# Performance work log

Hardware: AMD Instinct MI355X
Metric: run time of the kernel (lower is better)

Reference implementation:

```python
import jax, jax.numpy as jnp
import numpy as np

# Static ragged block structure: (num_graphs_in_bucket, n) -> block tensor (B, n, n, C)
BLOCKS = [(128, 32), (64, 48), (32, 64), (16, 96)]
C = 64
DEPTH = 2
EPS = 1e-5
N_TOTAL = sum(b * n * n for b, n in BLOCKS)  # 557056


def _mlp(h, w, b):
    # stack of DEPTH Linear(C->C) + ReLU layers (1x1 convs in the torch module)
    for d in range(w.shape[0]):
        h = jax.nn.relu(jnp.einsum('...i,oi->...o', h, w[d]) + b[d])
    return h


def _bn(h, g, b, m, v):
    # eval-mode BatchNorm1d with running stats
    return g * (h - m) * jax.lax.rsqrt(v + EPS) + b


def setup_inputs() -> dict:
    key = jax.random.key(0)
    ks = jax.random.split(key, 8)
    s = 1.0 / np.sqrt(C)

    def lin(k):
        return jax.random.normal(k, (C, C), jnp.float32) * s

    return dict(
        x=jax.random.normal(ks[0], (N_TOTAL, C), jnp.float32),
        w_m1=jax.random.normal(ks[1], (DEPTH, C, C), jnp.float32) * s,
        b_m1=jnp.zeros((DEPTH, C), jnp.float32),
        w_m2=jax.random.normal(ks[2], (DEPTH, C, C), jnp.float32) * s,
        b_m2=jnp.zeros((DEPTH, C), jnp.float32),
        W_skip=lin(ks[3]), b_skip=jnp.zeros((C,), jnp.float32),
        W_u1=lin(ks[4]), b_u1=jnp.zeros((C,), jnp.float32),
        g1=jnp.ones((C,), jnp.float32), beta1=jnp.zeros((C,), jnp.float32),
        rm1=jnp.zeros((C,), jnp.float32), rv1=jnp.ones((C,), jnp.float32),
        W_u2=lin(ks[5]), b_u2=jnp.zeros((C,), jnp.float32),
        g2=jnp.ones((C,), jnp.float32), beta2=jnp.zeros((C,), jnp.float32),
        rm2=jnp.zeros((C,), jnp.float32), rv2=jnp.ones((C,), jnp.float32),
    )


def reference(x, w_m1, b_m1, w_m2, b_m2, W_skip, b_skip,
              W_u1, b_u1, g1, beta1, rm1, rv1,
              W_u2, b_u2, g2, beta2, rm2, rv2):
    # --- ragged split -> per-block PPGN-style matmul conv -> cat ---
    hs = []
    off = 0
    for (bnum, n) in BLOCKS:
        ln = bnum * n * n
        blk = x[off:off + ln].reshape(bnum, n, n, C)  # (B, n, n, C)
        m1 = _mlp(blk, w_m1, b_m1)
        m2 = _mlp(blk, w_m2, b_m2)
        # per-channel spatial matmul over the n x n block
        h = jnp.einsum('bijc,bjkc->bikc', m1, m2)
        hs.append(h.reshape(ln, C))
        off += ln
    hs2 = jnp.concatenate(hs, 0) + (x @ W_skip.T + b_skip)
    # --- update MLP: Linear-BN-ReLU-(Dropout eval=id)-Linear-BN-ReLU + residual ---
    u = jax.nn.relu(_bn(hs2 @ W_u1.T + b_u1, g1, beta1, rm1, rv1))
    u = jax.nn.relu(_bn(u @ W_u2.T + b_u2, g2, beta2, rm2, rv2))
    return u + hs2
```

## Files before the change

kernel.cpp:

```cpp
#include <hip/hip_runtime.h>
#include <hip/hip_bf16.h>

#define NT 557056
typedef __hip_bfloat16 bf16;
typedef __attribute__((ext_vector_type(8))) short short8;
typedef __attribute__((ext_vector_type(4))) short short4v;
typedef __attribute__((ext_vector_type(4))) float f32x4;

__device__ __forceinline__ float b2f(bf16 v){ return __bfloat162float(v); }
__device__ __forceinline__ short f2bs(float f){ bf16 h = __float2bfloat16(f); return *(short*)&h; }
__device__ __forceinline__ float s2f(short s){ bf16 h = *(bf16*)&s; return __bfloat162float(h); }

__device__ __forceinline__ short8 ldfrag(const float* __restrict__ p){
  float4 a = *(const float4*)p;
  float4 b = *(const float4*)(p + 4);
  short8 r;
  r[0]=f2bs(a.x); r[1]=f2bs(a.y); r[2]=f2bs(a.z); r[3]=f2bs(a.w);
  r[4]=f2bs(b.x); r[5]=f2bs(b.y); r[6]=f2bs(b.z); r[7]=f2bs(b.w);
  return r;
}
#define MFMA(a,b,c) __builtin_amdgcn_mfma_f32_16x16x32_bf16(a, b, c, 0, 0, 0)

#define LS 72

__global__ __launch_bounds__(256) void k1_mlp(
    const float* __restrict__ x,
    const float* __restrict__ w_m1, const float* __restrict__ b_m1,
    const float* __restrict__ w_m2, const float* __restrict__ b_m2,
    bf16* __restrict__ m1t, bf16* __restrict__ m2t)
{
  __shared__ short yL[4][32][LS];
  const int tid = threadIdx.x;
  const int wv = tid >> 6, lane = tid & 63, r = lane & 15, g = lane >> 4;
  const int pbase = blockIdx.x * 128 + wv * 32;

  short8 xf[2][2];
  #pragma unroll
  for (int t = 0; t < 2; ++t)
    #pragma unroll
    for (int s = 0; s < 2; ++s)
      xf[t][s] = ldfrag(x + (size_t)(pbase + t*16 + r) * 64 + s*32 + g*8);

  for (int m = 0; m < 2; ++m) {
    const float* w0 = m ? w_m2 : w_m1;
    const float* b0 = m ? b_m2 : b_m1;
    const float* w1 = w0 + 4096;
    const float* b1 = b0 + 64;
    bf16* outp = m ? m2t : m1t;

    f32x4 acc[4][2];
    #pragma unroll
    for (int cb = 0; cb < 4; ++cb) {
      f32x4 bi = *(const f32x4*)(b0 + cb*16 + 4*g);
      acc[cb][0] = bi; acc[cb][1] = bi;
    }
    #pragma unroll
    for (int cb = 0; cb < 4; ++cb)
      #pragma unroll
      for (int s = 0; s < 2; ++s) {
        short8 wf = ldfrag(w0 + (cb*16 + r)*64 + s*32 + g*8);
        acc[cb][0] = MFMA(wf, xf[0][s], acc[cb][0]);
        acc[cb][1] = MFMA(wf, xf[1][s], acc[cb][1]);
      }
    __syncthreads();
    #pragma unroll
    for (int cb = 0; cb < 4; ++cb)
      #pragma unroll
      for (int t = 0; t < 2; ++t) {
        short4v v;
        #pragma unroll
        for (int q = 0; q < 4; ++q) v[q] = f2bs(fmaxf(acc[cb][t][q], 0.f));
        *(short4v*)&yL[wv][t*16 + r][cb*16 + 4*g] = v;
      }
    __syncthreads();

    f32x4 acc2[4][2];
    #pragma unroll
    for (int cb = 0; cb < 4; ++cb) {
      float bv = b1[cb*16 + r];
      f32x4 bi = {bv, bv, bv, bv};
      acc2[cb][0] = bi; acc2[cb][1] = bi;
    }
    short8 af[2][2];
    #pragma unroll
    for (int t = 0; t < 2; ++t)
      #pragma unroll
      for (int s = 0; s < 2; ++s)
        af[t][s] = *(const short8*)&yL[wv][t*16 + r][s*32 + g*8];
    #pragma unroll
    for (int cb = 0; cb < 4; ++cb)
      #pragma unroll
      for (int s = 0; s < 2; ++s) {
        short8 wf = ldfrag(w1 + (cb*16 + r)*64 + s*32 + g*8);
        acc2[cb][0] = MFMA(af[0][s], wf, acc2[cb][0]);
        acc2[cb][1] = MFMA(af[1][s], wf, acc2[cb][1]);
      }
    #pragma unroll
    for (int cb = 0; cb < 4; ++cb)
      #pragma unroll
      for (int t = 0; t < 2; ++t) {
        short4v v;
        #pragma unroll
        for (int q = 0; q < 4; ++q) v[q] = f2bs(fmaxf(acc2[cb][t][q], 0.f));
        *(short4v*)(outp + (size_t)(cb*16 + r) * NT + pbase + t*16 + 4*g) = v;
      }
  }
}

template<int N>
__global__ __launch_bounds__(256) void k2_spatial(
    const bf16* __restrict__ m1t, const bf16* __restrict__ m2t,
    bf16* __restrict__ ht, int off)
{
  constexpr int T = N / 16;
  __shared__ float A[N][N+1];
  __shared__ float B[N][N+1];
  const int b = blockIdx.x >> 6;
  const int c = blockIdx.x & 63;
  const size_t pbase = (size_t)c * NT + (size_t)off + (size_t)b * N * N;
  const int tid = threadIdx.x;

  for (int t8 = tid*8; t8 < N*N; t8 += 2048) {
    short8 v1 = *(const short8*)(m1t + pbase + t8);
    short8 v2 = *(const short8*)(m2t + pbase + t8);
    const int row = t8 / N, col = t8 - row*N;
    #pragma unroll
    for (int j = 0; j < 8; ++j) {
      A[row][col+j] = s2f(v1[j]);
      B[row][col+j] = s2f(v2[j]);
    }
  }
  __syncthreads();

  const int ti = tid >> 4, tk = tid & 15;
  float acc[T][T];
  #pragma unroll
  for (int ii = 0; ii < T; ++ii)
    #pragma unroll
    for (int kk = 0; kk < T; ++kk) acc[ii][kk] = 0.f;

  for (int j = 0; j < N; ++j) {
    float av[T], bv[T];
    #pragma unroll
    for (int ii = 0; ii < T; ++ii) av[ii] = A[ti*T+ii][j];
    #pragma unroll
    for (int kk = 0; kk < T; ++kk) bv[kk] = B[j][tk*T+kk];
    #pragma unroll
    for (int ii = 0; ii < T; ++ii)
      #pragma unroll
      for (int kk = 0; kk < T; ++kk)
        acc[ii][kk] = fmaf(av[ii], bv[kk], acc[ii][kk]);
  }

  #pragma unroll
  for (int ii = 0; ii < T; ++ii) {
    const int i = ti*T + ii;
    #pragma unroll
    for (int kk = 0; kk < T; ++kk)
      ht[pbase + i*N + tk*T + kk] = __float2bfloat16(acc[ii][kk]);
  }
}

__global__ __launch_bounds__(256) void k3_update(
    const float* __restrict__ x, const bf16* __restrict__ ht,
    const float* __restrict__ Wskip, const float* __restrict__ bskip,
    const float* __restrict__ Wu1, const float* __restrict__ bu1,
    const float* __restrict__ g1, const float* __restrict__ be1,
    const float* __restrict__ rm1, const float* __restrict__ rv1,
    const float* __restrict__ Wu2, const float* __restrict__ bu2,
    const float* __restrict__ g2, const float* __restrict__ be2,
    const float* __restrict__ rm2, const float* __restrict__ rv2,
    float* __restrict__ out)
{
  __shared__ short hs2L[4][32][LS];
  __shared__ short u1L[4][32][LS];
  const int tid = threadIdx.x;
  const int wv = tid >> 6, lane = tid & 63, r = lane & 15, g = lane >> 4;
  const int pbase = blockIdx.x * 128 + wv * 32;

  short8 xf[2][2];
  #pragma unroll
  for (int t = 0; t < 2; ++t)
    #pragma unroll
    for (int s = 0; s < 2; ++s)
      xf[t][s] = ldfrag(x + (size_t)(pbase + t*16 + r) * 64 + s*32 + g*8);

  f32x4 acc[4][2];
  #pragma unroll
  for (int cb = 0; cb < 4; ++cb) {
    float bv = bskip[cb*16 + r];
    f32x4 bi = {bv, bv, bv, bv};
    acc[cb][0] = bi; acc[cb][1] = bi;
  }
  #pragma unroll
  for (int cb = 0; cb < 4; ++cb)
    #pragma unroll
    for (int s = 0; s < 2; ++s) {
      short8 wf = ldfrag(Wskip + (cb*16 + r)*64 + s*32 + g*8);
      acc[cb][0] = MFMA(xf[0][s], wf, acc[cb][0]);
      acc[cb][1] = MFMA(xf[1][s], wf, acc[cb][1]);
    }
  #pragma unroll
  for (int cb = 0; cb < 4; ++cb)
    #pragma unroll
    for (int t = 0; t < 2; ++t) {
      short4v hv = *(const short4v*)(ht + (size_t)(cb*16 + r) * NT + pbase + t*16 + 4*g);
      #pragma unroll
      for (int q = 0; q < 4; ++q) acc[cb][t][q] += s2f(hv[q]);
    }
  __syncthreads();
  #pragma unroll
  for (int cb = 0; cb < 4; ++cb)
    #pragma unroll
    for (int t = 0; t < 2; ++t)
      #pragma unroll
      for (int q = 0; q < 4; ++q)
        hs2L[wv][t*16 + 4*g + q][cb*16 + r] = f2bs(acc[cb][t][q]);
  __syncthreads();

  f32x4 a1[4][2];
  #pragma unroll
  for (int cb = 0; cb < 4; ++cb) {
    f32x4 bi = *(const f32x4*)(bu1 + cb*16 + 4*g);
    a1[cb][0] = bi; a1[cb][1] = bi;
  }
  short8 hf[2][2];
  #pragma unroll
  for (int t = 0; t < 2; ++t)
    #pragma unroll
    for (int s = 0; s < 2; ++s)
      hf[t][s] = *(const short8*)&hs2L[wv][t*16 + r][s*32 + g*8];
  #pragma unroll
  for (int cb = 0; cb < 4; ++cb)
    #pragma unroll
    for (int s = 0; s < 2; ++s) {
      short8 wf = ldfrag(Wu1 + (cb*16 + r)*64 + s*32 + g*8);
      a1[cb][0] = MFMA(wf, hf[0][s], a1[cb][0]);
      a1[cb][1] = MFMA(wf, hf[1][s], a1[cb][1]);
    }
  #pragma unroll
  for (int cb = 0; cb < 4; ++cb) {
    f32x4 gg = *(const f32x4*)(g1  + cb*16 + 4*g);
    f32x4 vv = *(const f32x4*)(rv1 + cb*16 + 4*g);
    f32x4 mm = *(const f32x4*)(rm1 + cb*16 + 4*g);
    f32x4 bb = *(const f32x4*)(be1 + cb*16 + 4*g);
    f32x4 sc, sh;
    #pragma unroll
    for (int q = 0; q < 4; ++q) { sc[q] = gg[q] * rsqrtf(vv[q] + 1e-5f); sh[q] = bb[q] - mm[q]*sc[q]; }
    #pragma unroll
    for (int t = 0; t < 2; ++t) {
      short4v v;
      #pragma unroll
      for (int q = 0; q < 4; ++q) v[q] = f2bs(fmaxf(a1[cb][t][q]*sc[q] + sh[q], 0.f));
      *(short4v*)&u1L[wv][t*16 + r][cb*16 + 4*g] = v;
    }
  }
  __syncthreads();

  f32x4 a2[4][2];
  #pragma unroll
  for (int cb = 0; cb < 4; ++cb) {
    f32x4 bi = *(const f32x4*)(bu2 + cb*16 + 4*g);
    a2[cb][0] = bi; a2[cb][1] = bi;
  }
  short8 uf[2][2];
  #pragma unroll
  for (int t = 0; t < 2; ++t)
    #pragma unroll
    for (int s = 0; s < 2; ++s)
      uf[t][s] = *(const short8*)&u1L[wv][t*16 + r][s*32 + g*8];
  #pragma unroll
  for (int cb = 0; cb < 4; ++cb)
    #pragma unroll
    for (int s = 0; s < 2; ++s) {
      short8 wf = ldfrag(Wu2 + (cb*16 + r)*64 + s*32 + g*8);
      a2[cb][0] = MFMA(wf, uf[0][s], a2[cb][0]);
      a2[cb][1] = MFMA(wf, uf[1][s], a2[cb][1]);
    }
  #pragma unroll
  for (int cb = 0; cb < 4; ++cb) {
    f32x4 gg = *(const f32x4*)(g2  + cb*16 + 4*g);
    f32x4 vv = *(const f32x4*)(rv2 + cb*16 + 4*g);
    f32x4 mm = *(const f32x4*)(rm2 + cb*16 + 4*g);
    f32x4 bb = *(const f32x4*)(be2 + cb*16 + 4*g);
    f32x4 sc, sh;
    #pragma unroll
    for (int q = 0; q < 4; ++q) { sc[q] = gg[q] * rsqrtf(vv[q] + 1e-5f); sh[q] = bb[q] - mm[q]*sc[q]; }
    #pragma unroll
    for (int t = 0; t < 2; ++t) {
      short4v hv = *(const short4v*)&hs2L[wv][t*16 + r][cb*16 + 4*g];
      f32x4 res;
      #pragma unroll
      for (int q = 0; q < 4; ++q)
        res[q] = fmaxf(a2[cb][t][q]*sc[q] + sh[q], 0.f) + s2f(hv[q]);
      *(f32x4*)(out + (size_t)(pbase + t*16 + r) * 64 + cb*16 + 4*g) = res;
    }
  }
}

extern "C" void kernel_launch(void* const* d_in, const int* in_sizes, int n_in,
                              void* d_out, int out_size, void* d_ws, size_t ws_size,
                              hipStream_t stream) {
  const float* x     = (const float*)d_in[0];
  const float* w_m1  = (const float*)d_in[1];
  const float* b_m1  = (const float*)d_in[2];
  const float* w_m2  = (const float*)d_in[3];
  const float* b_m2  = (const float*)d_in[4];
  const float* Wskip = (const float*)d_in[5];
  const float* bskip = (const float*)d_in[6];
  const float* Wu1   = (const float*)d_in[7];
  const float* bu1   = (const float*)d_in[8];
  const float* g1    = (const float*)d_in[9];
  const float* be1   = (const float*)d_in[10];
  const float* rm1   = (const float*)d_in[11];
  const float* rv1   = (const float*)d_in[12];
  const float* Wu2   = (const float*)d_in[13];
  const float* bu2   = (const float*)d_in[14];
  const float* g2    = (const float*)d_in[15];
  const float* be2   = (const float*)d_in[16];
  const float* rm2   = (const float*)d_in[17];
  const float* rv2   = (const float*)d_in[18];
  float* out = (float*)d_out;

  bf16* m1t = (bf16*)d_ws;
  bf16* m2t = m1t + (size_t)64 * NT;
  bf16* ht  = m1t;

  k1_mlp<<<NT/128, 256, 0, stream>>>(x, w_m1, b_m1, w_m2, b_m2, m1t, m2t);

  k2_spatial<32><<<128*64, 256, 0, stream>>>(m1t, m2t, ht, 0);
  k2_spatial<48><<< 64*64, 256, 0, stream>>>(m1t, m2t, ht, 131072);
  k2_spatial<64><<< 32*64, 256, 0, stream>>>(m1t, m2t, ht, 278528);
  k2_spatial<96><<< 16*64, 256, 0, stream>>>(m1t, m2t, ht, 409600);

  k3_update<<<NT/128, 256, 0, stream>>>(x, ht, Wskip, bskip,
                                        Wu1, bu1, g1, be1, rm1, rv1,
                                        Wu2, bu2, g2, be2, rm2, rv2, out);
}
```

Measured before the change: 617.2 us.

## Persistent weight-resident MLP kernels with x prefetch and vectorized spatial matmul LDS

k1 and k3 become persistent kernels with 512 blocks. Each wave loads all weight fragments into registers once and loops over 17 tiles of 16 rows, prefetching the next x tile. Barriers are replaced by per-wave lgkmcnt waits, and BN scale/shift is folded with the bias. In k2, A is stored transposed in LDS so each thread can read vectorized float2/float4 operands, and outputs are written as packed bf16. The trade-off is much higher register pressure, fewer blocks, and bank conflicts from the transposed A writes.

```diff
diff --git a/kernel.cpp b/kernel.cpp
--- a/kernel.cpp
+++ b/kernel.cpp
@@ -11,99 +11,113 @@
 __device__ __forceinline__ short f2bs(float f){ bf16 h = __float2bfloat16(f); return *(short*)&h; }
 __device__ __forceinline__ float s2f(short s){ bf16 h = *(bf16*)&s; return __bfloat162float(h); }
 
-__device__ __forceinline__ short8 ldfrag(const float* __restrict__ p){
-  float4 a = *(const float4*)p;
-  float4 b = *(const float4*)(p + 4);
+__device__ __forceinline__ short8 cvt8(float4 a, float4 b){
   short8 r;
   r[0]=f2bs(a.x); r[1]=f2bs(a.y); r[2]=f2bs(a.z); r[3]=f2bs(a.w);
   r[4]=f2bs(b.x); r[5]=f2bs(b.y); r[6]=f2bs(b.z); r[7]=f2bs(b.w);
   return r;
 }
+__device__ __forceinline__ short8 ldfrag(const float* __restrict__ p){
+  return cvt8(*(const float4*)p, *(const float4*)(p + 4));
+}
 #define MFMA(a,b,c) __builtin_amdgcn_mfma_f32_16x16x32_bf16(a, b, c, 0, 0, 0)
-
-#define LS 72
-
-__global__ __launch_bounds__(256) void k1_mlp(
+#define LGKM0() asm volatile("s_waitcnt lgkmcnt(0)" ::: "memory")
+
+__global__ __launch_bounds__(256, 2) void k1_mlp(
     const float* __restrict__ x,
     const float* __restrict__ w_m1, const float* __restrict__ b_m1,
     const float* __restrict__ w_m2, const float* __restrict__ b_m2,
     bf16* __restrict__ m1t, bf16* __restrict__ m2t)
 {
-  __shared__ short yL[4][32][LS];
+  __shared__ short yL[4][16][72];
   const int tid = threadIdx.x;
   const int wv = tid >> 6, lane = tid & 63, r = lane & 15, g = lane >> 4;
-  const int pbase = blockIdx.x * 128 + wv * 32;
-
-  short8 xf[2][2];
-  #pragma unroll
-  for (int t = 0; t < 2; ++t)
-    #pragma unroll
-    for (int s = 0; s < 2; ++s)
-      xf[t][s] = ldfrag(x + (size_t)(pbase + t*16 + r) * 64 + s*32 + g*8);
-
+  const int wid = blockIdx.x * 4 + wv;
+
+  short8 wf[4][4][2];
+  {
+    const float* wp0 = w_m1;         const float* wp1 = w_m1 + 4096;
+    const float* wp2 = w_m2;         const float* wp3 = w_m2 + 4096;
+    #pragma unroll
+    for (int cb = 0; cb < 4; ++cb)
+      #pragma unroll
+      for (int s = 0; s < 2; ++s) {
+        const int o = (cb*16 + r)*64 + s*32 + g*8;
+        wf[0][cb][s] = ldfrag(wp0 + o);
+        wf[1][cb][s] = ldfrag(wp1 + o);
+        wf[2][cb][s] = ldfrag(wp2 + o);
+        wf[3][cb][s] = ldfrag(wp3 + o);
+      }
+  }
+  f32x4 b0v[2][4];
+  float b1v[2][4];
+  #pragma unroll
   for (int m = 0; m < 2; ++m) {
-    const float* w0 = m ? w_m2 : w_m1;
-    const float* b0 = m ? b_m2 : b_m1;
-    const float* w1 = w0 + 4096;
-    const float* b1 = b0 + 64;
-    bf16* outp = m ? m2t : m1t;
-
-    f32x4 acc[4][2];
-    #pragma unroll
-    for (int cb = 0; cb < 4; ++cb) {
-      f32x4 bi = *(const f32x4*)(b0 + cb*16 + 4*g);
-      acc[cb][0] = bi; acc[cb][1] = bi;
-    }
-    #pragma unroll
-    for (int cb = 0; cb < 4; ++cb)
-      #pragma unroll
-      for (int s = 0; s < 2; ++s) {
-        short8 wf = ldfrag(w0 + (cb*16 + r)*64 + s*32 + g*8);
-        acc[cb][0] = MFMA(wf, xf[0][s], acc[cb][0]);
-        acc[cb][1] = MFMA(wf, xf[1][s], acc[cb][1]);
-      }
-    __syncthreads();
-    #pragma unroll
-    for (int cb = 0; cb < 4; ++cb)
-      #pragma unroll
-      for (int t = 0; t < 2; ++t) {
+    const float* bb = m ? b_m2 : b_m1;
+    #pragma unroll
+    for (int cb = 0; cb < 4; ++cb) {
+      b0v[m][cb] = *(const f32x4*)(bb + cb*16 + 4*g);
+      b1v[m][cb] = bb[64 + cb*16 + r];
+    }
+  }
+
+  size_t pb = (size_t)wid * (17*16);
+  const float* xp0 = x + (pb + r)*64 + g*8;
+  float4 xr0 = *(const float4*)(xp0);
+  float4 xr1 = *(const float4*)(xp0 + 4);
+  float4 xr2 = *(const float4*)(xp0 + 32);
+  float4 xr3 = *(const float4*)(xp0 + 36);
+
+  for (int t = 0; t < 17; ++t, pb += 16) {
+    short8 xf0 = cvt8(xr0, xr1);
+    short8 xf1 = cvt8(xr2, xr3);
+    if (t < 16) {
+      const float* xn = x + (pb + 16 + r)*64 + g*8;
+      xr0 = *(const float4*)(xn);
+      xr1 = *(const float4*)(xn + 4);
+      xr2 = *(const float4*)(xn + 32);
+      xr3 = *(const float4*)(xn + 36);
+    }
+    #pragma unroll
+    for (int m = 0; m < 2; ++m) {
+      f32x4 acc[4];
+      #pragma unroll
+      for (int cb = 0; cb < 4; ++cb) acc[cb] = b0v[m][cb];
+      #pragma unroll
+      for (int cb = 0; cb < 4; ++cb) {
+        acc[cb] = MFMA(wf[2*m][cb][0], xf0, acc[cb]);
+        acc[cb] = MFMA(wf[2*m][cb][1], xf1, acc[cb]);
+      }
+      #pragma unroll
+      for (int cb = 0; cb < 4; ++cb) {
         short4v v;
         #pragma unroll
-        for (int q = 0; q < 4; ++q) v[q] = f2bs(fmaxf(acc[cb][t][q], 0.f));
-        *(short4v*)&yL[wv][t*16 + r][cb*16 + 4*g] = v;
-      }
-    __syncthreads();
-
-    f32x4 acc2[4][2];
-    #pragma unroll
-    for (int cb = 0; cb < 4; ++cb) {
-      float bv = b1[cb*16 + r];
-      f32x4 bi = {bv, bv, bv, bv};
-      acc2[cb][0] = bi; acc2[cb][1] = bi;
-    }
-    short8 af[2][2];
-    #pragma unroll
-    for (int t = 0; t < 2; ++t)
-      #pragma unroll
-      for (int s = 0; s < 2; ++s)
-        af[t][s] = *(const short8*)&yL[wv][t*16 + r][s*32 + g*8];
-    #pragma unroll
-    for (int cb = 0; cb < 4; ++cb)
-      #pragma unroll
-      for (int s = 0; s < 2; ++s) {
-        short8 wf = ldfrag(w1 + (cb*16 + r)*64 + s*32 + g*8);
-        acc2[cb][0] = MFMA(af[0][s], wf, acc2[cb][0]);
-        acc2[cb][1] = MFMA(af[1][s], wf, acc2[cb][1]);
-      }
-    #pragma unroll
-    for (int cb = 0; cb < 4; ++cb)
-      #pragma unroll
-      for (int t = 0; t < 2; ++t) {
+        for (int q = 0; q < 4; ++q) v[q] = f2bs(fmaxf(acc[cb][q], 0.f));
+        *(short4v*)&yL[wv][r][cb*16 + 4*g] = v;
+      }
+      LGKM0();
+      short8 a0 = *(const short8*)&yL[wv][r][g*8];
+      short8 a1 = *(const short8*)&yL[wv][r][32 + g*8];
+      f32x4 acc2[4];
+      #pragma unroll
+      for (int cb = 0; cb < 4; ++cb) {
+        const float bv = b1v[m][cb];
+        acc2[cb] = (f32x4){bv, bv, bv, bv};
+      }
+      #pragma unroll
+      for (int cb = 0; cb < 4; ++cb) {
+        acc2[cb] = MFMA(a0, wf[2*m+1][cb][0], acc2[cb]);
+        acc2[cb] = MFMA(a1, wf[2*m+1][cb][1], acc2[cb]);
+      }
+      bf16* op = m ? m2t : m1t;
+      #pragma unroll
+      for (int cb = 0; cb < 4; ++cb) {
         short4v v;
         #pragma unroll
-        for (int q = 0; q < 4; ++q) v[q] = f2bs(fmaxf(acc2[cb][t][q], 0.f));
-        *(short4v*)(outp + (size_t)(cb*16 + r) * NT + pbase + t*16 + 4*g) = v;
-      }
+        for (int q = 0; q < 4; ++q) v[q] = f2bs(fmaxf(acc2[cb][q], 0.f));
+        *(short4v*)(op + (size_t)(cb*16 + r) * NT + pb + 4*g) = v;
+      }
+    }
   }
 }
 
@@ -113,22 +127,24 @@
     bf16* __restrict__ ht, int off)
 {
   constexpr int T = N / 16;
-  __shared__ float A[N][N+1];
-  __shared__ float B[N][N+1];
+  constexpr int SA = N + 4;
+  __shared__ __align__(16) float AT[N*SA];
+  __shared__ __align__(16) float Bs[N*SA];
   const int b = blockIdx.x >> 6;
   const int c = blockIdx.x & 63;
   const size_t pbase = (size_t)c * NT + (size_t)off + (size_t)b * N * N;
   const int tid = threadIdx.x;
 
-  for (int t8 = tid*8; t8 < N*N; t8 += 2048) {
-    short8 v1 = *(const short8*)(m1t + pbase + t8);
-    short8 v2 = *(const short8*)(m2t + pbase + t8);
-    const int row = t8 / N, col = t8 - row*N;
-    #pragma unroll
-    for (int j = 0; j < 8; ++j) {
-      A[row][col+j] = s2f(v1[j]);
-      B[row][col+j] = s2f(v2[j]);
-    }
+  for (int idx = tid*4; idx < N*N; idx += 1024) {
+    short4v a4 = *(const short4v*)(m1t + pbase + idx);
+    short4v b4 = *(const short4v*)(m2t + pbase + idx);
+    const int j = idx / N, k0 = idx - j*N;
+    f32x4 bf;
+    #pragma unroll
+    for (int q = 0; q < 4; ++q) bf[q] = s2f(b4[q]);
+    *(f32x4*)&Bs[j*SA + k0] = bf;
+    #pragma unroll
+    for (int q = 0; q < 4; ++q) AT[(k0+q)*SA + j] = s2f(a4[q]);
   }
   __syncthreads();
 
@@ -140,11 +156,25 @@
     for (int kk = 0; kk < T; ++kk) acc[ii][kk] = 0.f;
 
   for (int j = 0; j < N; ++j) {
+    const float* ar = &AT[j*SA + ti*T];
+    const float* br = &Bs[j*SA + tk*T];
     float av[T], bv[T];
-    #pragma unroll
-    for (int ii = 0; ii < T; ++ii) av[ii] = A[ti*T+ii][j];
-    #pragma unroll
-    for (int kk = 0; kk < T; ++kk) bv[kk] = B[j][tk*T+kk];
+    if constexpr (T == 2) {
+      float2 a2 = *(const float2*)ar; av[0]=a2.x; av[1]=a2.y;
+      float2 b2 = *(const float2*)br; bv[0]=b2.x; bv[1]=b2.y;
+    } else if constexpr (T == 3) {
+      av[0]=ar[0]; av[1]=ar[1]; av[2]=ar[2];
+      bv[0]=br[0]; bv[1]=br[1]; bv[2]=br[2];
+    } else if constexpr (T == 4) {
+      float4 a4 = *(const float4*)ar; av[0]=a4.x; av[1]=a4.y; av[2]=a4.z; av[3]=a4.w;
+      float4 b4 = *(const float4*)br; bv[0]=b4.x; bv[1]=b4.y; bv[2]=b4.z; bv[3]=b4.w;
+    } else {
+      #pragma unroll
+      for (int p = 0; p < 3; ++p) {
+        float2 a2 = *(const float2*)(ar + 2*p); av[2*p]=a2.x; av[2*p+1]=a2.y;
+        float2 b2 = *(const float2*)(br + 2*p); bv[2*p]=b2.x; bv[2*p+1]=b2.y;
+      }
+    }
     #pragma unroll
     for (int ii = 0; ii < T; ++ii)
       #pragma unroll
@@ -154,14 +184,29 @@
 
   #pragma unroll
   for (int ii = 0; ii < T; ++ii) {
-    const int i = ti*T + ii;
-    #pragma unroll
-    for (int kk = 0; kk < T; ++kk)
-      ht[pbase + i*N + tk*T + kk] = __float2bfloat16(acc[ii][kk]);
-  }
-}
-
-__global__ __launch_bounds__(256) void k3_update(
+    const int row = ti*T + ii;
+    bf16* dst = ht + pbase + row*N + tk*T;
+    unsigned short tmp[T];
+    #pragma unroll
+    for (int kk = 0; kk < T; ++kk) tmp[kk] = (unsigned short)f2bs(acc[ii][kk]);
+    if constexpr (T == 2) {
+      *(unsigned int*)dst = (unsigned int)tmp[0] | ((unsigned int)tmp[1] << 16);
+    } else if constexpr (T == 3) {
+      ((unsigned short*)dst)[0] = tmp[0];
+      ((unsigned short*)dst)[1] = tmp[1];
+      ((unsigned short*)dst)[2] = tmp[2];
+    } else if constexpr (T == 4) {
+      short4v v; v[0]=(short)tmp[0]; v[1]=(short)tmp[1]; v[2]=(short)tmp[2]; v[3]=(short)tmp[3];
+      *(short4v*)dst = v;
+    } else {
+      #pragma unroll
+      for (int p = 0; p < 3; ++p)
+        *((unsigned int*)dst + p) = (unsigned int)tmp[2*p] | ((unsigned int)tmp[2*p+1] << 16);
+    }
+  }
+}
+
+__global__ __launch_bounds__(256, 2) void k3_update(
     const float* __restrict__ x, const bf16* __restrict__ ht,
     const float* __restrict__ Wskip, const float* __restrict__ bskip,
     const float* __restrict__ Wu1, const float* __restrict__ bu1,
@@ -172,128 +217,122 @@
     const float* __restrict__ rm2, const float* __restrict__ rv2,
     float* __restrict__ out)
 {
-  __shared__ short hs2L[4][32][LS];
-  __shared__ short u1L[4][32][LS];
+  __shared__ short hs2L[4][16][88];
+  __shared__ short u1L[4][16][72];
   const int tid = threadIdx.x;
   const int wv = tid >> 6, lane = tid & 63, r = lane & 15, g = lane >> 4;
-  const int pbase = blockIdx.x * 128 + wv * 32;
-
-  short8 xf[2][2];
-  #pragma unroll
-  for (int t = 0; t < 2; ++t)
-    #pragma unroll
-    for (int s = 0; s < 2; ++s)
-      xf[t][s] = ldfrag(x + (size_t)(pbase + t*16 + r) * 64 + s*32 + g*8);
-
-  f32x4 acc[4][2];
+  const int wid = blockIdx.x * 4 + wv;
+
+  short8 wsk[4][2], w1f[4][2], w2f[4][2];
+  #pragma unroll
+  for (int cb = 0; cb < 4; ++cb)
+    #pragma unroll
+    for (int s = 0; s < 2; ++s) {
+      const int o = (cb*16 + r)*64 + s*32 + g*8;
+      wsk[cb][s] = ldfrag(Wskip + o);
+      w1f[cb][s] = ldfrag(Wu1 + o);
+      w2f[cb][s] = ldfrag(Wu2 + o);
+    }
+  float bskv[4];
+  f32x4 sc1v[4], sh1v[4], sc2v[4], sh2v[4];
   #pragma unroll
   for (int cb = 0; cb < 4; ++cb) {
-    float bv = bskip[cb*16 + r];
-    f32x4 bi = {bv, bv, bv, bv};
-    acc[cb][0] = bi; acc[cb][1] = bi;
-  }
-  #pragma unroll
-  for (int cb = 0; cb < 4; ++cb)
-    #pragma unroll
-    for (int s = 0; s < 2; ++s) {
-      short8 wf = ldfrag(Wskip + (cb*16 + r)*64 + s*32 + g*8);
-      acc[cb][0] = MFMA(xf[0][s], wf, acc[cb][0]);
-      acc[cb][1] = MFMA(xf[1][s], wf, acc[cb][1]);
-    }
-  #pragma unroll
-  for (int cb = 0; cb < 4; ++cb)
-    #pragma unroll
-    for (int t = 0; t < 2; ++t) {
-      short4v hv = *(const short4v*)(ht + (size_t)(cb*16 + r) * NT + pbase + t*16 + 4*g);
-      #pragma unroll
-      for (int q = 0; q < 4; ++q) acc[cb][t][q] += s2f(hv[q]);
-    }
-  __syncthreads();
-  #pragma unroll
-  for (int cb = 0; cb < 4; ++cb)
-    #pragma unroll
-    for (int t = 0; t < 2; ++t)
+    bskv[cb] = bskip[cb*16 + r];
+    const int o = cb*16 + 4*g;
+    f32x4 gg1 = *(const f32x4*)(g1 + o),  vv1 = *(const f32x4*)(rv1 + o);
+    f32x4 mm1 = *(const f32x4*)(rm1 + o), bb1 = *(const f32x4*)(be1 + o);
+    f32x4 bu1v = *(const f32x4*)(bu1 + o);
+    f32x4 gg2 = *(const f32x4*)(g2 + o),  vv2 = *(const f32x4*)(rv2 + o);
+    f32x4 mm2 = *(const f32x4*)(rm2 + o), bb2 = *(const f32x4*)(be2 + o);
+    f32x4 bu2v = *(const f32x4*)(bu2 + o);
+    #pragma unroll
+    for (int q = 0; q < 4; ++q) {
+      const float s1 = gg1[q] * rsqrtf(vv1[q] + 1e-5f);
+      sc1v[cb][q] = s1; sh1v[cb][q] = bb1[q] + (bu1v[q] - mm1[q]) * s1;
+      const float s2 = gg2[q] * rsqrtf(vv2[q] + 1e-5f);
+      sc2v[cb][q] = s2; sh2v[cb][q] = bb2[q] + (bu2v[q] - mm2[q]) * s2;
+    }
+  }
+
+  size_t pb = (size_t)wid * (17*16);
+  const float* xp0 = x + (pb + r)*64 + g*8;
+  float4 xr0 = *(const float4*)(xp0);
+  float4 xr1 = *(const float4*)(xp0 + 4);
+  float4 xr2 = *(const float4*)(xp0 + 32);
+  float4 xr3 = *(const float4*)(xp0 + 36);
+
+  for (int t = 0; t < 17; ++t, pb += 16) {
+    short8 xf0 = cvt8(xr0, xr1);
+    short8 xf1 = cvt8(xr2, xr3);
+    if (t < 16) {
+      const float* xn = x + (pb + 16 + r)*64 + g*8;
+      xr0 = *(const float4*)(xn);
+      xr1 = *(const float4*)(xn + 4);
+      xr2 = *(const float4*)(xn + 32);
+      xr3 = *(const float4*)(xn + 36);
+    }
+    short4v hv[4];
+    #pragma unroll
+    for (int cb = 0; cb < 4; ++cb)
+      hv[cb] = *(const short4v*)(ht + (size_t)(cb*16 + r) * NT + pb + 4*g);
+
+    f32x4 acc[4];
+    #pragma unroll
+    for (int cb = 0; cb < 4; ++cb) acc[cb] = (f32x4){bskv[cb], bskv[cb], bskv[cb], bskv[cb]};
+    #pragma unroll
+    for (int cb = 0; cb < 4; ++cb) {
+      acc[cb] = MFMA(xf0, wsk[cb][0], acc[cb]);
+      acc[cb] = MFMA(xf1, wsk[cb][1], acc[cb]);
+    }
+    #pragma unroll
+    for (int cb = 0; cb < 4; ++cb)
+      #pragma unroll
+      for (int q = 0; q < 4; ++q) acc[cb][q] += s2f(hv[cb][q]);
+    #pragma unroll
+    for (int cb = 0; cb < 4; ++cb)
       #pragma unroll
       for (int q = 0; q < 4; ++q)
-        hs2L[wv][t*16 + 4*g + q][cb*16 + r] = f2bs(acc[cb][t][q]);
-  __syncthreads();
-
-  f32x4 a1[4][2];
-  #pragma unroll
-  for (int cb = 0; cb < 4; ++cb) {
-    f32x4 bi = *(const f32x4*)(bu1 + cb*16 + 4*g);
-    a1[cb][0] = bi; a1[cb][1] = bi;
-  }
-  short8 hf[2][2];
-  #pragma unroll
-  for (int t = 0; t < 2; ++t)
-    #pragma unroll
-    for (int s = 0; s < 2; ++s)
-      hf[t][s] = *(const short8*)&hs2L[wv][t*16 + r][s*32 + g*8];
-  #pragma unroll
-  for (int cb = 0; cb < 4; ++cb)
-    #pragma unroll
-    for (int s = 0; s < 2; ++s) {
-      short8 wf = ldfrag(Wu1 + (cb*16 + r)*64 + s*32 + g*8);
-      a1[cb][0] = MFMA(wf, hf[0][s], a1[cb][0]);
-      a1[cb][1] = MFMA(wf, hf[1][s], a1[cb][1]);
-    }
-  #pragma unroll
-  for (int cb = 0; cb < 4; ++cb) {
-    f32x4 gg = *(const f32x4*)(g1  + cb*16 + 4*g);
-    f32x4 vv = *(const f32x4*)(rv1 + cb*16 + 4*g);
-    f32x4 mm = *(const f32x4*)(rm1 + cb*16 + 4*g);
-    f32x4 bb = *(const f32x4*)(be1 + cb*16 + 4*g);
-    f32x4 sc, sh;
-    #pragma unroll
-    for (int q = 0; q < 4; ++q) { sc[q] = gg[q] * rsqrtf(vv[q] + 1e-5f); sh[q] = bb[q] - mm[q]*sc[q]; }
-    #pragma unroll
-    for (int t = 0; t < 2; ++t) {
+        hs2L[wv][4*g + q][cb*16 + r] = f2bs(acc[cb][q]);
+    LGKM0();
+    short8 h0 = *(const short8*)&hs2L[wv][r][g*8];
+    short8 h1 = *(const short8*)&hs2L[wv][r][32 + g*8];
+
+    f32x4 a1[4];
+    #pragma unroll
+    for (int cb = 0; cb < 4; ++cb) a1[cb] = (f32x4){0.f, 0.f, 0.f, 0.f};
+    #pragma unroll
+    for (int cb = 0; cb < 4; ++cb) {
+      a1[cb] = MFMA(w1f[cb][0], h0, a1[cb]);
+      a1[cb] = MFMA(w1f[cb][1], h1, a1[cb]);
+    }
+    #pragma unroll
+    for (int cb = 0; cb < 4; ++cb) {
       short4v v;
       #pragma unroll
-      for (int q = 0; q < 4; ++q) v[q] = f2bs(fmaxf(a1[cb][t][q]*sc[q] + sh[q], 0.f));
-      *(short4v*)&u1L[wv][t*16 + r][cb*16 + 4*g] = v;
-    }
-  }
-  __syncthreads();
-
-  f32x4 a2[4][2];
-  #pragma unroll
-  for (int cb = 0; cb < 4; ++cb) {
-    f32x4 bi = *(const f32x4*)(bu2 + cb*16 + 4*g);
-    a2[cb][0] = bi; a2[cb][1] = bi;
-  }
-  short8 uf[2][2];
-  #pragma unroll
-  for (int t = 0; t < 2; ++t)
-    #pragma unroll
-    for (int s = 0; s < 2; ++s)
-      uf[t][s] = *(const short8*)&u1L[wv][t*16 + r][s*32 + g*8];
-  #pragma unroll
-  for (int cb = 0; cb < 4; ++cb)
-    #pragma unroll
-    for (int s = 0; s < 2; ++s) {
-      short8 wf = ldfrag(Wu2 + (cb*16 + r)*64 + s*32 + g*8);
-      a2[cb][0] = MFMA(wf, uf[0][s], a2[cb][0]);
-      a2[cb][1] = MFMA(wf, uf[1][s], a2[cb][1]);
-    }
-  #pragma unroll
-  for (int cb = 0; cb < 4; ++cb) {
-    f32x4 gg = *(const f32x4*)(g2  + cb*16 + 4*g);
-    f32x4 vv = *(const f32x4*)(rv2 + cb*16 + 4*g);
-    f32x4 mm = *(const f32x4*)(rm2 + cb*16 + 4*g);
-    f32x4 bb = *(const f32x4*)(be2 + cb*16 + 4*g);
-    f32x4 sc, sh;
-    #pragma unroll
-    for (int q = 0; q < 4; ++q) { sc[q] = gg[q] * rsqrtf(vv[q] + 1e-5f); sh[q] = bb[q] - mm[q]*sc[q]; }
-    #pragma unroll
-    for (int t = 0; t < 2; ++t) {
-      short4v hv = *(const short4v*)&hs2L[wv][t*16 + r][cb*16 + 4*g];
+      for (int q = 0; q < 4; ++q)
+        v[q] = f2bs(fmaxf(a1[cb][q]*sc1v[cb][q] + sh1v[cb][q], 0.f));
+      *(short4v*)&u1L[wv][r][cb*16 + 4*g] = v;
+    }
+    LGKM0();
+    short8 u0 = *(const short8*)&u1L[wv][r][g*8];
+    short8 u1f = *(const short8*)&u1L[wv][r][32 + g*8];
+
+    f32x4 a2[4];
+    #pragma unroll
+    for (int cb = 0; cb < 4; ++cb) a2[cb] = (f32x4){0.f, 0.f, 0.f, 0.f};
+    #pragma unroll
+    for (int cb = 0; cb < 4; ++cb) {
+      a2[cb] = MFMA(w2f[cb][0], u0, a2[cb]);
+      a2[cb] = MFMA(w2f[cb][1], u1f, a2[cb]);
+    }
+    #pragma unroll
+    for (int cb = 0; cb < 4; ++cb) {
+      short4v hres = *(const short4v*)&hs2L[wv][r][cb*16 + 4*g];
       f32x4 res;
       #pragma unroll
       for (int q = 0; q < 4; ++q)
-        res[q] = fmaxf(a2[cb][t][q]*sc[q] + sh[q], 0.f) + s2f(hv[q]);
-      *(f32x4*)(out + (size_t)(pbase + t*16 + r) * 64 + cb*16 + 4*g) = res;
+        res[q] = fmaxf(a2[cb][q]*sc2v[cb][q] + sh2v[cb][q], 0.f) + s2f(hres[q]);
+      *(f32x4*)(out + (pb + r)*64 + cb*16 + 4*g) = res;
     }
   }
 }
@@ -326,14 +365,14 @@
   bf16* m2t = m1t + (size_t)64 * NT;
   bf16* ht  = m1t;
 
-  k1_mlp<<<NT/128, 256, 0, stream>>>(x, w_m1, b_m1, w_m2, b_m2, m1t, m2t);
+  k1_mlp<<<512, 256, 0, stream>>>(x, w_m1, b_m1, w_m2, b_m2, m1t, m2t);
 
   k2_spatial<32><<<128*64, 256, 0, stream>>>(m1t, m2t, ht, 0);
   k2_spatial<48><<< 64*64, 256, 0, stream>>>(m1t, m2t, ht, 131072);
   k2_spatial<64><<< 32*64, 256, 0, stream>>>(m1t, m2t, ht, 278528);
   k2_spatial<96><<< 16*64, 256, 0, stream>>>(m1t, m2t, ht, 409600);
 
-  k3_update<<<NT/128, 256, 0, stream>>>(x, ht, Wskip, bskip,
-                                        Wu1, bu1, g1, be1, rm1, rv1,
-                                        Wu2, bu2, g2, be2, rm2, rv2, out);
-}
+  k3_update<<<512, 256, 0, stream>>>(x, ht, Wskip, bskip,
+                                     Wu1, bu1, g1, be1, rm1, rv1,
+                                     Wu2, bu2, g2, be2, rm2, rv2, out);
+}
```

Result: faster. 566.2 us (-8.3%).
